# Kernel tuning notes

Hardware: AMD Instinct MI355X
Metric: run time of the kernel (lower is better)

Reference implementation:

```python
import jax, jax.numpy as jnp
import numpy as np

FEAT_DIM = 512
NUM_CLASSES = 50000
ALPHA = 0.1
BATCH = 8192


def setup_inputs() -> dict:
    key = jax.random.key(0)
    k1, k2, k3 = jax.random.split(key, 3)
    features = jax.random.normal(k1, (BATCH, FEAT_DIM), dtype=jnp.float32)
    labels = jax.random.randint(k2, (BATCH,), 0, NUM_CLASSES, dtype=jnp.int64)
    centers = jax.random.normal(k3, (NUM_CLASSES, FEAT_DIM), dtype=jnp.float32)
    return {"features": features, "labels": labels, "centers": centers}


def reference(features, labels, centers):
    # --- center loss: gather centers, squared L2, mean over batch ---
    batch_centers = centers[labels]                       # [B, D]
    diff = features - batch_centers
    center_loss = jnp.sum(diff * diff, axis=1).mean()

    # --- training-mode EMA center update (fused segment-mean, replaces per-class loop) ---
    num_classes = centers.shape[0]
    counts = jax.ops.segment_sum(
        jnp.ones((features.shape[0],), dtype=features.dtype), labels,
        num_segments=num_classes)                         # [C]
    sums = jax.ops.segment_sum(features, labels, num_segments=num_classes)  # [C, D]
    present = counts > 0
    safe_counts = jnp.where(present, counts, 1.0)
    class_means = sums / safe_counts[:, None]             # [C, D]
    delta = jnp.where(present[:, None],
                      (class_means - centers) * ALPHA,
                      0.0)
    new_centers = centers + delta

    return center_loss, new_centers
```

## Files before the change

kernel.cpp:

```cpp
#include <hip/hip_runtime.h>

constexpr int FEAT = 512;
constexpr int NCLS = 50000;
constexpr int B    = 8192;
constexpr float ALPHA_F = 0.1f;
constexpr int NBINS = 256;


__global__ void k_init(int* __restrict__ head, float* __restrict__ bins) {
    int i = blockIdx.x * blockDim.x + threadIdx.x;
    if (i < NCLS) head[i] = -1;
    if (i < NBINS) bins[i] = 0.0f;
}

__global__ void k_build(const int* __restrict__ labels,
                        int* __restrict__ head, int* __restrict__ next) {
    int i = blockIdx.x * blockDim.x + threadIdx.x;
    if (i < B) next[i] = atomicExch(&head[labels[i]], i);
}

__global__ void __launch_bounds__(256)
k_class(const float* __restrict__ centers,
        const float* __restrict__ features,
        const int* __restrict__ head,
        const int* __restrict__ next,
        float* __restrict__ out,
        float* __restrict__ bins) {
    const int wid  = (int)((blockIdx.x * 256 + threadIdx.x) >> 6);
    const int lane = threadIdx.x & 63;
    if (wid >= NCLS) return;

    const float4* c4 = (const float4*)(centers + (size_t)wid * FEAT);
    const float4 a0 = c4[lane];
    const float4 a1 = c4[lane + 64];

    float4 S0 = make_float4(0.f, 0.f, 0.f, 0.f);
    float4 S1 = make_float4(0.f, 0.f, 0.f, 0.f);
    float loss = 0.0f;
    int cnt = 0;
    int j = __builtin_amdgcn_readfirstlane(head[wid]);
    while (j >= 0) {
        const float4* f4 = (const float4*)(features + (size_t)j * FEAT);
        const float4 f0 = f4[lane];
        const float4 f1 = f4[lane + 64];
        S0.x += f0.x; S0.y += f0.y; S0.z += f0.z; S0.w += f0.w;
        S1.x += f1.x; S1.y += f1.y; S1.z += f1.z; S1.w += f1.w;
        float d;
        d = f0.x - a0.x; loss += d * d;
        d = f0.y - a0.y; loss += d * d;
        d = f0.z - a0.z; loss += d * d;
        d = f0.w - a0.w; loss += d * d;
        d = f1.x - a1.x; loss += d * d;
        d = f1.y - a1.y; loss += d * d;
        d = f1.z - a1.z; loss += d * d;
        d = f1.w - a1.w; loss += d * d;
        j = __builtin_amdgcn_readfirstlane(next[j]);
        ++cnt;
    }

    float4 n0, n1;
    if (cnt > 0) {
        const float s = 1.0f - ALPHA_F;
        const float w = ALPHA_F / (float)cnt;
        n0 = make_float4(a0.x * s + S0.x * w, a0.y * s + S0.y * w,
                         a0.z * s + S0.z * w, a0.w * s + S0.w * w);
        n1 = make_float4(a1.x * s + S1.x * w, a1.y * s + S1.y * w,
                         a1.z * s + S1.z * w, a1.w * s + S1.w * w);
    } else {
        n0 = a0; n1 = a1;
    }

#pragma unroll
    for (int off = 32; off > 0; off >>= 1)
        loss += __shfl_down(loss, off);
    if (lane == 0 && cnt > 0) atomicAdd(&bins[wid & (NBINS - 1)], loss);

    float* orow = out + 1 + (size_t)wid * FEAT;
    const float bx = __shfl(n1.x, 0);
    const float by = __shfl(n1.y, 0);
    const float bz = __shfl(n1.z, 0);
    float x0 = __shfl_down(n0.x, 1), y0 = __shfl_down(n0.y, 1), z0 = __shfl_down(n0.z, 1);
    float x1 = __shfl_down(n1.x, 1), y1 = __shfl_down(n1.y, 1), z1 = __shfl_down(n1.z, 1);
    if (lane == 63) { x0 = bx; y0 = by; z0 = bz; }

    if (lane == 0) { orow[0] = n0.x; orow[1] = n0.y; orow[2] = n0.z; }
    float4* oa = (float4*)(orow + 3);
    oa[lane] = make_float4(n0.w, x0, y0, z0);
    if (lane < 63)
        oa[64 + lane] = make_float4(n1.w, x1, y1, z1);
    if (lane == 63) orow[511] = n1.w;
}

__global__ void k_fin(const float* __restrict__ bins, float* __restrict__ out) {
    const int t = threadIdx.x;
    float s = bins[t];
#pragma unroll
    for (int off = 32; off > 0; off >>= 1)
        s += __shfl_down(s, off);
    __shared__ float sm[4];
    if ((t & 63) == 0) sm[t >> 6] = s;
    __syncthreads();
    if (t == 0) out[0] = (sm[0] + sm[1] + sm[2] + sm[3]) / (float)B;
}

extern "C" void kernel_launch(void* const* d_in, const int* in_sizes, int n_in,
                              void* d_out, int out_size, void* d_ws, size_t ws_size,
                              hipStream_t stream) {
    const float* features = (const float*)d_in[0];
    const int*   labels   = (const int*)d_in[1];
    const float* centers  = (const float*)d_in[2];

    float* out  = (float*)d_out;
    int*   head = (int*)d_ws;
    int*   next = head + NCLS;
    float* bins = (float*)(next + B);

    k_init<<<(NCLS + 255) / 256, 256, 0, stream>>>(head, bins);
    k_build<<<(B + 255) / 256, 256, 0, stream>>>(labels, head, next);
    k_class<<<(NCLS + 3) / 4, 256, 0, stream>>>(centers, features, head, next, out, bins);
    k_fin<<<1, 256, 0, stream>>>(bins, out);
}
```

Before: 47.84 us.

## Process two classes per wavefront, use nontemporal output stores, vectorize head init

Each wavefront now handles two consecutive classes, loading both center rows and both list heads up front so more memory requests are in flight per wave, with half as many waves launched. Output rows are written with nontemporal stores so the 100MB streaming output does not pollute cache. The head array init is written with int4 stores. The trade-offs are more registers per wave, lower wave count, and serialized traversal of the two linked lists.

```diff
diff --git a/kernel.cpp b/kernel.cpp
--- a/kernel.cpp
+++ b/kernel.cpp
@@ -6,10 +6,12 @@
 constexpr float ALPHA_F = 0.1f;
 constexpr int NBINS = 256;
 
+typedef float f32x4 __attribute__((ext_vector_type(4)));
+
 
 __global__ void k_init(int* __restrict__ head, float* __restrict__ bins) {
     int i = blockIdx.x * blockDim.x + threadIdx.x;
-    if (i < NCLS) head[i] = -1;
+    if (i < NCLS / 4) ((int4*)head)[i] = make_int4(-1, -1, -1, -1);
     if (i < NBINS) bins[i] = 0.0f;
 }
 
@@ -19,6 +21,28 @@
     if (i < B) next[i] = atomicExch(&head[labels[i]], i);
 }
 
+__device__ __forceinline__ void store_row(float* __restrict__ orow,
+                                          float4 n0, float4 n1, int lane) {
+    const float bx = __shfl(n1.x, 0);
+    const float by = __shfl(n1.y, 0);
+    const float bz = __shfl(n1.z, 0);
+    float x0 = __shfl_down(n0.x, 1), y0 = __shfl_down(n0.y, 1), z0 = __shfl_down(n0.z, 1);
+    float x1 = __shfl_down(n1.x, 1), y1 = __shfl_down(n1.y, 1), z1 = __shfl_down(n1.z, 1);
+    if (lane == 63) { x0 = bx; y0 = by; z0 = bz; }
+
+    if (lane == 0) {
+        __builtin_nontemporal_store(n0.x, orow + 0);
+        __builtin_nontemporal_store(n0.y, orow + 1);
+        __builtin_nontemporal_store(n0.z, orow + 2);
+    }
+    f32x4* oa = (f32x4*)(orow + 3);
+    __builtin_nontemporal_store((f32x4){n0.w, x0, y0, z0}, oa + lane);
+    if (lane < 63)
+        __builtin_nontemporal_store((f32x4){n1.w, x1, y1, z1}, oa + 64 + lane);
+    if (lane == 63)
+        __builtin_nontemporal_store(n1.w, orow + 511);
+}
+
 __global__ void __launch_bounds__(256)
 k_class(const float* __restrict__ centers,
         const float* __restrict__ features,
@@ -26,69 +50,79 @@
         const int* __restrict__ next,
         float* __restrict__ out,
         float* __restrict__ bins) {
-    const int wid  = (int)((blockIdx.x * 256 + threadIdx.x) >> 6);
+    const int w    = (int)((blockIdx.x * 256 + threadIdx.x) >> 6);
     const int lane = threadIdx.x & 63;
-    if (wid >= NCLS) return;
+    const int cA   = w * 2;
+    if (cA >= NCLS) return;
+    const int cB   = cA + 1;
 
-    const float4* c4 = (const float4*)(centers + (size_t)wid * FEAT);
-    const float4 a0 = c4[lane];
-    const float4 a1 = c4[lane + 64];
+    const float4* cA4 = (const float4*)(centers + (size_t)cA * FEAT);
+    const float4* cB4 = (const float4*)(centers + (size_t)cB * FEAT);
+    const float4 aA0 = cA4[lane];
+    const float4 aA1 = cA4[lane + 64];
+    const float4 aB0 = cB4[lane];
+    const float4 aB1 = cB4[lane + 64];
+    const int hA = __builtin_amdgcn_readfirstlane(head[cA]);
+    const int hB = __builtin_amdgcn_readfirstlane(head[cB]);
 
-    float4 S0 = make_float4(0.f, 0.f, 0.f, 0.f);
-    float4 S1 = make_float4(0.f, 0.f, 0.f, 0.f);
+    float4 SA0 = {0,0,0,0}, SA1 = {0,0,0,0};
+    float4 SB0 = {0,0,0,0}, SB1 = {0,0,0,0};
     float loss = 0.0f;
-    int cnt = 0;
-    int j = __builtin_amdgcn_readfirstlane(head[wid]);
-    while (j >= 0) {
+    int cntA = 0, cntB = 0;
+
+    for (int j = hA; j >= 0; j = __builtin_amdgcn_readfirstlane(next[j]), ++cntA) {
         const float4* f4 = (const float4*)(features + (size_t)j * FEAT);
         const float4 f0 = f4[lane];
         const float4 f1 = f4[lane + 64];
-        S0.x += f0.x; S0.y += f0.y; S0.z += f0.z; S0.w += f0.w;
-        S1.x += f1.x; S1.y += f1.y; S1.z += f1.z; S1.w += f1.w;
+        SA0.x += f0.x; SA0.y += f0.y; SA0.z += f0.z; SA0.w += f0.w;
+        SA1.x += f1.x; SA1.y += f1.y; SA1.z += f1.z; SA1.w += f1.w;
         float d;
-        d = f0.x - a0.x; loss += d * d;
-        d = f0.y - a0.y; loss += d * d;
-        d = f0.z - a0.z; loss += d * d;
-        d = f0.w - a0.w; loss += d * d;
-        d = f1.x - a1.x; loss += d * d;
-        d = f1.y - a1.y; loss += d * d;
-        d = f1.z - a1.z; loss += d * d;
-        d = f1.w - a1.w; loss += d * d;
-        j = __builtin_amdgcn_readfirstlane(next[j]);
-        ++cnt;
+        d = f0.x - aA0.x; loss += d * d;
+        d = f0.y - aA0.y; loss += d * d;
+        d = f0.z - aA0.z; loss += d * d;
+        d = f0.w - aA0.w; loss += d * d;
+        d = f1.x - aA1.x; loss += d * d;
+        d = f1.y - aA1.y; loss += d * d;
+        d = f1.z - aA1.z; loss += d * d;
+        d = f1.w - aA1.w; loss += d * d;
+    }
+    for (int j = hB; j >= 0; j = __builtin_amdgcn_readfirstlane(next[j]), ++cntB) {
+        const float4* f4 = (const float4*)(features + (size_t)j * FEAT);
+        const float4 f0 = f4[lane];
+        const float4 f1 = f4[lane + 64];
+        SB0.x += f0.x; SB0.y += f0.y; SB0.z += f0.z; SB0.w += f0.w;
+        SB1.x += f1.x; SB1.y += f1.y; SB1.z += f1.z; SB1.w += f1.w;
+        float d;
+        d = f0.x - aB0.x; loss += d * d;
+        d = f0.y - aB0.y; loss += d * d;
+        d = f0.z - aB0.z; loss += d * d;
+        d = f0.w - aB0.w; loss += d * d;
+        d = f1.x - aB1.x; loss += d * d;
+        d = f1.y - aB1.y; loss += d * d;
+        d = f1.z - aB1.z; loss += d * d;
+        d = f1.w - aB1.w; loss += d * d;
     }
 
-    float4 n0, n1;
-    if (cnt > 0) {
-        const float s = 1.0f - ALPHA_F;
-        const float w = ALPHA_F / (float)cnt;
-        n0 = make_float4(a0.x * s + S0.x * w, a0.y * s + S0.y * w,
-                         a0.z * s + S0.z * w, a0.w * s + S0.w * w);
-        n1 = make_float4(a1.x * s + S1.x * w, a1.y * s + S1.y * w,
-                         a1.z * s + S1.z * w, a1.w * s + S1.w * w);
-    } else {
-        n0 = a0; n1 = a1;
-    }
+    float4 nA0, nA1, nB0, nB1;
+    if (cntA > 0) {
+        const float s = 1.0f - ALPHA_F, v = ALPHA_F / (float)cntA;
+        nA0 = make_float4(aA0.x*s + SA0.x*v, aA0.y*s + SA0.y*v, aA0.z*s + SA0.z*v, aA0.w*s + SA0.w*v);
+        nA1 = make_float4(aA1.x*s + SA1.x*v, aA1.y*s + SA1.y*v, aA1.z*s + SA1.z*v, aA1.w*s + SA1.w*v);
+    } else { nA0 = aA0; nA1 = aA1; }
+    if (cntB > 0) {
+        const float s = 1.0f - ALPHA_F, v = ALPHA_F / (float)cntB;
+        nB0 = make_float4(aB0.x*s + SB0.x*v, aB0.y*s + SB0.y*v, aB0.z*s + SB0.z*v, aB0.w*s + SB0.w*v);
+        nB1 = make_float4(aB1.x*s + SB1.x*v, aB1.y*s + SB1.y*v, aB1.z*s + SB1.z*v, aB1.w*s + SB1.w*v);
+    } else { nB0 = aB0; nB1 = aB1; }
 
 #pragma unroll
     for (int off = 32; off > 0; off >>= 1)
         loss += __shfl_down(loss, off);
-    if (lane == 0 && cnt > 0) atomicAdd(&bins[wid & (NBINS - 1)], loss);
+    if (lane == 0 && (cntA + cntB) > 0)
+        atomicAdd(&bins[w & (NBINS - 1)], loss);
 
-    float* orow = out + 1 + (size_t)wid * FEAT;
-    const float bx = __shfl(n1.x, 0);
-    const float by = __shfl(n1.y, 0);
-    const float bz = __shfl(n1.z, 0);
-    float x0 = __shfl_down(n0.x, 1), y0 = __shfl_down(n0.y, 1), z0 = __shfl_down(n0.z, 1);
-    float x1 = __shfl_down(n1.x, 1), y1 = __shfl_down(n1.y, 1), z1 = __shfl_down(n1.z, 1);
-    if (lane == 63) { x0 = bx; y0 = by; z0 = bz; }
-
-    if (lane == 0) { orow[0] = n0.x; orow[1] = n0.y; orow[2] = n0.z; }
-    float4* oa = (float4*)(orow + 3);
-    oa[lane] = make_float4(n0.w, x0, y0, z0);
-    if (lane < 63)
-        oa[64 + lane] = make_float4(n1.w, x1, y1, z1);
-    if (lane == 63) orow[511] = n1.w;
+    store_row(out + 1 + (size_t)cA * FEAT, nA0, nA1, lane);
+    store_row(out + 1 + (size_t)cB * FEAT, nB0, nB1, lane);
 }
 
 __global__ void k_fin(const float* __restrict__ bins, float* __restrict__ out) {
@@ -115,8 +149,8 @@
     int*   next = head + NCLS;
     float* bins = (float*)(next + B);
 
-    k_init<<<(NCLS + 255) / 256, 256, 0, stream>>>(head, bins);
+    k_init<<<(NCLS / 4 + 255) / 256, 256, 0, stream>>>(head, bins);
     k_build<<<(B + 255) / 256, 256, 0, stream>>>(labels, head, next);
-    k_class<<<(NCLS + 3) / 4, 256, 0, stream>>>(centers, features, head, next, out, bins);
+    k_class<<<(NCLS / 2 + 3) / 4, 256, 0, stream>>>(centers, features, head, next, out, bins);
     k_fin<<<1, 256, 0, stream>>>(bins, out);
 }
```

New measurement: 48.90 us. 1.02x slower.
